# Performance work log

Measured on AMD Instinct MI355X. Metric: run time of the kernel, lower is better.

The kernel has to match this reference:

```python
import jax, jax.numpy as jnp
import numpy as np

EPS = 1e-5
NHEAD = 8
TOP_K = 2


def _layernorm(x, g, b):
    m = jnp.mean(x, axis=-1, keepdims=True)
    v = jnp.mean((x - m) ** 2, axis=-1, keepdims=True)
    return (x - m) * jax.lax.rsqrt(v + EPS) * g + b


def setup_inputs() -> dict:
    S, D, F, E = 4096, 512, 2048, 8
    key = jax.random.key(0)
    ks = jax.random.split(key, 18)
    std = 0.02
    return {
        "src": jax.random.normal(ks[0], (S, D), jnp.float32),
        "in_proj_w": std * jax.random.normal(ks[1], (3 * D, D), jnp.float32),
        "in_proj_b": jnp.zeros((3 * D,), jnp.float32),
        "out_proj_w": std * jax.random.normal(ks[2], (D, D), jnp.float32),
        "out_proj_b": jnp.zeros((D,), jnp.float32),
        "ln1_g": jnp.ones((D,), jnp.float32),
        "ln1_b": jnp.zeros((D,), jnp.float32),
        "ln2_g": jnp.ones((D,), jnp.float32),
        "ln2_b": jnp.zeros((D,), jnp.float32),
        "gate_w": std * jax.random.normal(ks[3], (E, D), jnp.float32),
        "gate_b": jnp.zeros((E,), jnp.float32),
        "w1": std * jax.random.normal(ks[4], (E, F, D), jnp.float32),
        "b1": jnp.zeros((E, F), jnp.float32),
        "w2": std * jax.random.normal(ks[5], (E, F, D), jnp.float32),
        "b2": jnp.zeros((E, F), jnp.float32),
        "wo": std * jax.random.normal(ks[6], (E, D, F), jnp.float32),
        "bo": jnp.zeros((E, D), jnp.float32),
    }


def _sa_block(x, in_proj_w, in_proj_b, out_proj_w, out_proj_b):
    # x: [S, D] unbatched sequence (torch MultiheadAttention unbatched path)
    S, D = x.shape
    hd = D // NHEAD
    qkv = x @ in_proj_w.T + in_proj_b              # [S, 3D]
    q, k, v = jnp.split(qkv, 3, axis=-1)
    q = q.reshape(S, NHEAD, hd)
    k = k.reshape(S, NHEAD, hd)
    v = v.reshape(S, NHEAD, hd)
    scores = jnp.einsum("shd,thd->hst", q, k) / jnp.sqrt(jnp.float32(hd))
    attn = jax.nn.softmax(scores, axis=-1)         # [H, S, S]
    out = jnp.einsum("hst,thd->shd", attn, v).reshape(S, D)
    return out @ out_proj_w.T + out_proj_b


def _ff_block(x, gate_w, gate_b, w1, b1, w2, b2, wo, bo):
    # top-k gated SwiGLU MoE; gate probs are softmax, NOT renormalized after topk
    T = x.shape[0]
    E = w1.shape[0]
    gates = jax.nn.softmax(x @ gate_w.T + gate_b, axis=-1)      # [T, E]
    top_scores, top_idx = jax.lax.top_k(gates, TOP_K)            # [T, k]
    combine = jnp.zeros((T, E), x.dtype).at[
        jnp.arange(T)[:, None], top_idx].add(top_scores)         # [T, E]
    out = jnp.zeros_like(x)
    for e in range(E):  # small fixed expert count
        h = jax.nn.silu(x @ w1[e].T + b1[e]) * (x @ w2[e].T + b2[e])
        out = out + combine[:, e:e + 1] * (h @ wo[e].T + bo[e])
    return out


def reference(src, in_proj_w, in_proj_b, out_proj_w, out_proj_b,
              ln1_g, ln1_b, ln2_g, ln2_b,
              gate_w, gate_b, w1, b1, w2, b2, wo, bo):
    # norm_first pre-norm residual layer, dropout=0 (eval)
    x = src
    x = x + _sa_block(_layernorm(x, ln1_g, ln1_b),
                      in_proj_w, in_proj_b, out_proj_w, out_proj_b)
    x = x + _ff_block(_layernorm(x, ln2_g, ln2_b),
                      gate_w, gate_b, w1, b1, w2, b2, wo, bo)
    return x
```

## Files before the change

kernel.cpp:

```cpp
#include <hip/hip_runtime.h>
#include <hip/hip_bf16.h>
#include <math.h>

#define SQ   4096
#define DM   512
#define NH   8
#define HDIM 64
#define FF   2048
#define NE   8

typedef unsigned short u16;
typedef unsigned int   u32;
typedef __attribute__((ext_vector_type(8))) __bf16 bf16x8;
typedef __attribute__((ext_vector_type(4))) float  f32x4;

__device__ __forceinline__ float bf2f(u16 v) {
    union { u32 i; float f; } c; c.i = ((u32)v) << 16; return c.f;
}
__device__ __forceinline__ u16 f2bf(float f) {
    union { __bf16 h; u16 u; } c; c.h = (__bf16)f; return c.u;
}

#define BM 128
#define BN 128
#define BK 32
#define BKP 40

__global__ __launch_bounds__(256) void gemm_split(
    const u16* __restrict__ Ahi, const u16* __restrict__ Alo, int lda,
    const u16* __restrict__ Bhi, const u16* __restrict__ Blo, int ldb,
    int M, int N, int K,
    const float* __restrict__ bias,
    const float* __restrict__ resid, int ldres,
    u16* __restrict__ Chi, u16* __restrict__ Clo,
    float* __restrict__ Cf, int ldc, int mode)
{
    __shared__ __align__(16) u16 Ash[BM * BKP], Asl[BM * BKP];
    __shared__ __align__(16) u16 Bsh[BN * BKP], Bsl[BN * BKP];
    const int tid  = threadIdx.x;
    const int wave = tid >> 6;
    const int lane = tid & 63;
    const int quad = lane >> 4;
    const int l16  = lane & 15;
    const int bm = blockIdx.x * BM;
    const int bn = blockIdx.y * BN;
    const int wm = (wave & 1) * 64;
    const int wn = (wave >> 1) * 64;

    f32x4 acc[4][4];
#pragma unroll
    for (int i = 0; i < 4; i++)
#pragma unroll
        for (int j = 0; j < 4; j++)
#pragma unroll
            for (int r = 0; r < 4; r++) acc[i][j][r] = 0.0f;

    for (int k0 = 0; k0 < K; k0 += BK) {
#pragma unroll
        for (int i = 0; i < 2; i++) {
            int c = tid + i * 256;
            int row = c >> 2;
            int col = (c & 3) << 3;
            int ga = bm + row, gb2 = bn + row;
            uint4 vah = make_uint4(0u,0u,0u,0u), val = vah, vbh = vah, vbl = vah;
            if (ga < M) {
                vah = *(const uint4*)(Ahi + (size_t)ga * lda + k0 + col);
                val = *(const uint4*)(Alo + (size_t)ga * lda + k0 + col);
            }
            if (gb2 < N) {
                vbh = *(const uint4*)(Bhi + (size_t)gb2 * ldb + k0 + col);
                vbl = *(const uint4*)(Blo + (size_t)gb2 * ldb + k0 + col);
            }
            *(uint4*)(Ash + row * BKP + col) = vah;
            *(uint4*)(Asl + row * BKP + col) = val;
            *(uint4*)(Bsh + row * BKP + col) = vbh;
            *(uint4*)(Bsl + row * BKP + col) = vbl;
        }
        __syncthreads();
        bf16x8 ah[4], al[4], bh[4], bl[4];
#pragma unroll
    for (int i = 0; i < 4; i++) {
            ah[i] = *(const bf16x8*)(Ash + (wm + i * 16 + l16) * BKP + quad * 8);
            al[i] = *(const bf16x8*)(Asl + (wm + i * 16 + l16) * BKP + quad * 8);
        }
#pragma unroll
        for (int j = 0; j < 4; j++) {
            bh[j] = *(const bf16x8*)(Bsh + (wn + j * 16 + l16) * BKP + quad * 8);
            bl[j] = *(const bf16x8*)(Bsl + (wn + j * 16 + l16) * BKP + quad * 8);
        }
#pragma unroll
        for (int i = 0; i < 4; i++)
#pragma unroll
            for (int j = 0; j < 4; j++) {
                acc[i][j] = __builtin_amdgcn_mfma_f32_16x16x32_bf16(ah[i], bh[j], acc[i][j], 0,0,0);
                acc[i][j] = __builtin_amdgcn_mfma_f32_16x16x32_bf16(ah[i], bl[j], acc[i][j], 0,0,0);
                acc[i][j] = __builtin_amdgcn_mfma_f32_16x16x32_bf16(al[i], bh[j], acc[i][j], 0,0,0);
            }
        __syncthreads();
    }

#pragma unroll
    for (int i = 0; i < 4; i++)
#pragma unroll
        for (int j = 0; j < 4; j++)
#pragma unroll
            for (int r = 0; r < 4; r++) {
                int row = bm + wm + i * 16 + quad * 4 + r;
                int col = bn + wn + j * 16 + l16;
                if (row >= M || col >= N) continue;
                float v = acc[i][j][r] + (bias ? bias[col] : 0.0f);
                size_t idx = (size_t)row * ldc + col;
                if (mode == 0) {
                    u16 hb = f2bf(v);
                    Chi[idx] = hb;
                    Clo[idx] = f2bf(v - bf2f(hb));
                } else {
                    if (resid) v += resid[(size_t)row * ldres + col];
                    Cf[idx] = v;
                }
            }
}

__global__ __launch_bounds__(256) void gemm_split_ko(
    const u16* __restrict__ Ahi, const u16* __restrict__ Alo, int lda,
    const u16* __restrict__ Bhi, const u16* __restrict__ Blo, int ldb,
    float* __restrict__ Cf, int ldc)
{
    __shared__ __align__(16) u16 Ash[BM * BKP], Asl[BM * BKP];
    __shared__ __align__(16) u16 Bsh[BN * BKP], Bsl[BN * BKP];
    const int tid  = threadIdx.x;
    const int wave = tid >> 6;
    const int lane = tid & 63;
    const int quad = lane >> 4;
    const int l16  = lane & 15;
    const int bm = blockIdx.x * BM;
    const int bn = blockIdx.y * BN;
    const int wm = (wave & 1) * 64;
    const int wn = (wave >> 1) * 64;
    const int KC    = DM / 4;
    const int k0beg = blockIdx.z * KC;

    f32x4 acc[4][4];
#pragma unroll
    for (int i = 0; i < 4; i++)
#pragma unroll
        for (int j = 0; j < 4; j++)
#pragma unroll
            for (int r = 0; r < 4; r++) acc[i][j][r] = 0.0f;

    for (int k0 = k0beg; k0 < k0beg + KC; k0 += BK) {
#pragma unroll
        for (int i = 0; i < 2; i++) {
            int c = tid + i * 256;
            int row = c >> 2;
            int col = (c & 3) << 3;
            int ga = bm + row, gb2 = bn + row;
            uint4 vah = *(const uint4*)(Ahi + (size_t)ga * lda + k0 + col);
            uint4 val = *(const uint4*)(Alo + (size_t)ga * lda + k0 + col);
            uint4 vbh = *(const uint4*)(Bhi + (size_t)gb2 * ldb + k0 + col);
            uint4 vbl = *(const uint4*)(Blo + (size_t)gb2 * ldb + k0 + col);
            *(uint4*)(Ash + row * BKP + col) = vah;
            *(uint4*)(Asl + row * BKP + col) = val;
            *(uint4*)(Bsh + row * BKP + col) = vbh;
            *(uint4*)(Bsl + row * BKP + col) = vbl;
        }
        __syncthreads();
        bf16x8 ah[4], al[4], bh[4], bl[4];
#pragma unroll
        for (int i = 0; i < 4; i++) {
            ah[i] = *(const bf16x8*)(Ash + (wm + i * 16 + l16) * BKP + quad * 8);
            al[i] = *(const bf16x8*)(Asl + (wm + i * 16 + l16) * BKP + quad * 8);
        }
#pragma unroll
        for (int j = 0; j < 4; j++) {
            bh[j] = *(const bf16x8*)(Bsh + (wn + j * 16 + l16) * BKP + quad * 8);
            bl[j] = *(const bf16x8*)(Bsl + (wn + j * 16 + l16) * BKP + quad * 8);
        }
#pragma unroll
        for (int i = 0; i < 4; i++)
#pragma unroll
            for (int j = 0; j < 4; j++) {
                acc[i][j] = __builtin_amdgcn_mfma_f32_16x16x32_bf16(ah[i], bh[j], acc[i][j], 0,0,0);
                acc[i][j] = __builtin_amdgcn_mfma_f32_16x16x32_bf16(ah[i], bl[j], acc[i][j], 0,0,0);
                acc[i][j] = __builtin_amdgcn_mfma_f32_16x16x32_bf16(al[i], bh[j], acc[i][j], 0,0,0);
            }
        __syncthreads();
    }

#pragma unroll
    for (int i = 0; i < 4; i++)
#pragma unroll
        for (int j = 0; j < 4; j++)
#pragma unroll
            for (int r = 0; r < 4; r++) {
                int row = bm + wm + i * 16 + quad * 4 + r;
                int col = bn + wn + j * 16 + l16;
                atomicAdd(Cf + (size_t)row * ldc + col, acc[i][j][r]);
            }
}

__global__ __launch_bounds__(256) void init_x1(
    const float* __restrict__ src, const float* __restrict__ bias,
    float* __restrict__ x1)
{
    int i = blockIdx.x * 256 + threadIdx.x;
    int col4 = i & (DM / 4 - 1);
    float4 s = ((const float4*)src)[i];
    float4 b = ((const float4*)bias)[col4];
    s.x += b.x; s.y += b.y; s.z += b.z; s.w += b.w;
    ((float4*)x1)[i] = s;
}

__global__ __launch_bounds__(256) void moe12_all(
    const u16* __restrict__ A, int lda,
    const int* __restrict__ idxl, const int* __restrict__ cnt,
    const int* __restrict__ off,
    const float* __restrict__ w1, const float* __restrict__ b1,
    const float* __restrict__ w2, const float* __restrict__ b2,
    u16* __restrict__ H)
{
    const int bmg = blockIdx.x * BM;
    if (bmg >= off[NE]) return;
    int e = 0;
    while (e < NE - 1 && bmg >= off[e + 1]) e++;
    const int M   = cnt[e];
    const int bml = bmg - off[e];
    if (bml >= M) return;
    const float* B1 = w1 + (size_t)e * FF * DM;
    const float* B2 = w2 + (size_t)e * FF * DM;
    const int*   rl = idxl + e * SQ;

    __shared__ __align__(16) u16 As[BM * BKP], Bs1[BN * BKP], Bs2[BN * BKP];
    const int tid  = threadIdx.x;
    const int wave = tid >> 6;
// ... 194 lines not shown

    f32x4 acc[4][4];
#pragma unroll
    for (int i = 0; i < 4; i++)
#pragma unroll
        for (int j = 0; j < 4; j++)
#pragma unroll
            for (int r = 0; r < 4; r++) acc[i][j][r] = 0.0f;

    for (int k0 = 0; k0 < FF; k0 += BK) {
#pragma unroll
        for (int i = 0; i < 2; i++) {
            int c = tid + i * 256;
            int row = c >> 2;
            int col = (c & 3) << 3;
            uint4 va = *(const uint4*)(H + (size_t)(bmg + row) * FF + k0 + col);
            *(uint4*)(As + row * BKP + col) = va;
        }
#pragma unroll
        for (int i = 0; i < 4; i++) {
            int c = tid + i * 256;
            int row = c >> 3;
            int col = (c & 7) << 2;
            float4 v = *(const float4*)(B + (size_t)(bn + row) * FF + k0 + col);
            ushort4 h;
            h.x = f2bf(v.x); h.y = f2bf(v.y); h.z = f2bf(v.z); h.w = f2bf(v.w);
            *(ushort4*)(Bs + row * BKP + col) = h;
        }
        __syncthreads();
        bf16x8 af[4], bf[4];
#pragma unroll
        for (int i = 0; i < 4; i++)
            af[i] = *(const bf16x8*)(As + (wm + i * 16 + l16) * BKP + quad * 8);
#pragma unroll
        for (int j = 0; j < 4; j++)
            bf[j] = *(const bf16x8*)(Bs + (wn + j * 16 + l16) * BKP + quad * 8);
#pragma unroll
        for (int i = 0; i < 4; i++)
#pragma unroll
            for (int j = 0; j < 4; j++)
                acc[i][j] = __builtin_amdgcn_mfma_f32_16x16x32_bf16(af[i], bf[j], acc[i][j], 0,0,0);
        __syncthreads();
    }

#pragma unroll
    for (int i = 0; i < 4; i++)
#pragma unroll
        for (int j = 0; j < 4; j++)
#pragma unroll
            for (int r = 0; r < 4; r++) {
                int rowl = bml + wm + i * 16 + quad * 4 + r;
                if (rowl >= M) continue;
                int col = bn + wn + j * 16 + l16;
                int tok = idxl[e * SQ + rowl];
                float wgt = cw[e * SQ + rowl];
                atomicAdd(out + (size_t)tok * DM + col,
                          wgt * (acc[i][j][r] + bo[e * DM + col]));
            }
}

__global__ __launch_bounds__(256) void moe_y_bf16(
    const u16* __restrict__ H,
    const u16* __restrict__ wob, const float* __restrict__ bo,
    const int* __restrict__ idxl, const float* __restrict__ cw,
    const int* __restrict__ cnt, const int* __restrict__ off,
    float* __restrict__ out)
{
    const int bmg = blockIdx.x * BM;
    if (bmg >= off[NE]) return;
    int e = 0;
    while (e < NE - 1 && bmg >= off[e + 1]) e++;
    const int M   = cnt[e];
    const int bml = bmg - off[e];
    if (bml >= M) return;
    const u16* B = wob + (size_t)e * DM * FF;

    __shared__ __align__(16) u16 As[BM * BKP], Bs[BN * BKP];
    const int tid  = threadIdx.x;
    const int wave = tid >> 6;
    const int lane = tid & 63;
    const int quad = lane >> 4;
    const int l16  = lane & 15;
    const int bn = blockIdx.y * BN;
    const int wm = (wave & 1) * 64;
    const int wn = (wave >> 1) * 64;

    f32x4 acc[4][4];
#pragma unroll
    for (int i = 0; i < 4; i++)
#pragma unroll
        for (int j = 0; j < 4; j++)
#pragma unroll
            for (int r = 0; r < 4; r++) acc[i][j][r] = 0.0f;

    for (int k0 = 0; k0 < FF; k0 += BK) {
#pragma unroll
        for (int i = 0; i < 2; i++) {
            int c = tid + i * 256;
            int row = c >> 2;
            int col = (c & 3) << 3;
            uint4 va = *(const uint4*)(H + (size_t)(bmg + row) * FF + k0 + col);
            *(uint4*)(As + row * BKP + col) = va;
            uint4 vb = *(const uint4*)(B + (size_t)(bn + row) * FF + k0 + col);
            *(uint4*)(Bs + row * BKP + col) = vb;
        }
        __syncthreads();
        bf16x8 af[4], bf[4];
#pragma unroll
        for (int i = 0; i < 4; i++)
            af[i] = *(const bf16x8*)(As + (wm + i * 16 + l16) * BKP + quad * 8);
#pragma unroll
        for (int j = 0; j < 4; j++)
            bf[j] = *(const bf16x8*)(Bs + (wn + j * 16 + l16) * BKP + quad * 8);
#pragma unroll
        for (int i = 0; i < 4; i++)
#pragma unroll
            for (int j = 0; j < 4; j++)
                acc[i][j] = __builtin_amdgcn_mfma_f32_16x16x32_bf16(af[i], bf[j], acc[i][j], 0,0,0);
        __syncthreads();
    }

#pragma unroll
    for (int i = 0; i < 4; i++)
#pragma unroll
        for (int j = 0; j < 4; j++)
#pragma unroll
            for (int r = 0; r < 4; r++) {
                int rowl = bml + wm + i * 16 + quad * 4 + r;
                if (rowl >= M) continue;
                int col = bn + wn + j * 16 + l16;
                int tok = idxl[e * SQ + rowl];
                float wgt = cw[e * SQ + rowl];
                atomicAdd(out + (size_t)tok * DM + col,
                          wgt * (acc[i][j][r] + bo[e * DM + col]));
            }
}

__global__ __launch_bounds__(256) void cvt_w_bf16(
    const float* __restrict__ w, u16* __restrict__ wb, int n4)
{
    int i = blockIdx.x * 256 + threadIdx.x;
    if (i < n4) {
        float4 v = ((const float4*)w)[i];
        ushort4 h;
        h.x = f2bf(v.x); h.y = f2bf(v.y); h.z = f2bf(v.z); h.w = f2bf(v.w);
        ((ushort4*)wb)[i] = h;
    }
}

#define KP 64
#define SWZ(row, col) ((col) ^ (((row) & 7) << 3))
#define SCL 0.18033688011112042f

template <int SPLIT>
__device__ __forceinline__ void flash_body(
    const u16* __restrict__ qh, const u16* __restrict__ ql,
    const u16* __restrict__ vth, const u16* __restrict__ vtl,
    u16* __restrict__ oh, u16* __restrict__ ol,
    float* __restrict__ Opart, float* __restrict__ mpart,
    float* __restrict__ lpart)
{
    __shared__ __align__(16) u16 Ksh[64*KP], Ksl[64*KP], Vsh[64*KP], Vsl[64*KP];
    const int tid  = threadIdx.x;
    const int wave = tid >> 6;
    const int lane = tid & 63;
    const int quad = lane >> 4;
    const int l16  = lane & 15;
    const int h    = blockIdx.y;
    const int z    = (SPLIT > 1) ? blockIdx.z : 0;
    const int qbase = blockIdx.x * 64 + wave * 16;

    const int r_st  = tid >> 3;
    const int co_g  = (tid & 7) << 3;
    const int co_sw = SWZ(r_st, co_g);

    bf16x8 aqh[2], aql[2];
#pragma unroll
    for (int kk = 0; kk < 2; kk++) {
        size_t off = (size_t)(qbase + l16) * (3*DM) + h*HDIM + kk*32 + quad*8;
        aqh[kk] = *(const bf16x8*)(qh + off);
        aql[kk] = *(const bf16x8*)(ql + off);
    }

    float m_ = -1e30f, l_ = 0.0f;
    f32x4 o_[4];
#pragma unroll
    for (int nd = 0; nd < 4; nd++)
#pragma unroll
        for (int r = 0; r < 4; r++) o_[nd][r] = 0.0f;

    const int srcA = l16 + ((quad & 1) * 2) * 16;
    const int srcB = srcA + 16;
    const bool hiJ = (quad >> 1);

    const int NT    = SQ / 64 / SPLIT;
    const int jtBeg = z * NT, jtEnd = (z + 1) * NT;

    for (int jt = jtBeg; jt < jtEnd; jt++) {
        {
            size_t koff0 = (size_t)(jt*64 + r_st) * (3*DM) + DM + h*HDIM + co_g;
            size_t voff0 = (size_t)(h*HDIM + r_st) * SQ + jt*64 + co_g;
            size_t koff1 = koff0 + (size_t)32 * (3*DM);
            size_t voff1 = voff0 + (size_t)32 * SQ;
            uint4 a0 = *(const uint4*)(qh  + koff0);
            uint4 a1 = *(const uint4*)(ql  + koff0);
            uint4 a2 = *(const uint4*)(vth + voff0);
            uint4 a3 = *(const uint4*)(vtl + voff0);
            uint4 b0 = *(const uint4*)(qh  + koff1);
            uint4 b1 = *(const uint4*)(ql  + koff1);
            uint4 b2 = *(const uint4*)(vth + voff1);
            uint4 b3 = *(const uint4*)(vtl + voff1);
            *(uint4*)(Ksh + r_st*KP + co_sw)      = a0;
            *(uint4*)(Ksl + r_st*KP + co_sw)      = a1;
            *(uint4*)(Vsh + r_st*KP + co_sw)      = a2;
            *(uint4*)(Vsl + r_st*KP + co_sw)      = a3;
            *(uint4*)(Ksh + (r_st+32)*KP + co_sw) = b0;
            *(uint4*)(Ksl + (r_st+32)*KP + co_sw) = b1;
            *(uint4*)(Vsh + (r_st+32)*KP + co_sw) = b2;
            *(uint4*)(Vsl + (r_st+32)*KP + co_sw) = b3;
        }
        __syncthreads();

        f32x4 s[4];
        __builtin_amdgcn_s_setprio(1);
#pragma unroll
        for (int jn = 0; jn < 4; jn++) {
            f32x4 zz;
#pragma unroll
            for (int r = 0; r < 4; r++) zz[r] = 0.0f;
#pragma unroll
            for (int kk = 0; kk < 2; kk++) {
                int krow = jn*16 + l16;
                int kcol = SWZ(krow, kk*32 + quad*8);
                bf16x8 kh = *(const bf16x8*)(Ksh + krow*KP + kcol);
                bf16x8 kl = *(const bf16x8*)(Ksl + krow*KP + kcol);
                zz = __builtin_amdgcn_mfma_f32_16x16x32_bf16(kh, aqh[kk], zz, 0,0,0);
                zz = __builtin_amdgcn_mfma_f32_16x16x32_bf16(kl, aqh[kk], zz, 0,0,0);
                zz = __builtin_amdgcn_mfma_f32_16x16x32_bf16(kh, aql[kk], zz, 0,0,0);
            }
#pragma unroll
            for (int r = 0; r < 4; r++) zz[r] *= SCL;
            s[jn] = zz;
        }
        __builtin_amdgcn_s_setprio(0);

        float mx = s[0][0];
#pragma unroll
        for (int jn = 0; jn < 4; jn++)
#pragma unroll
            for (int r = 0; r < 4; r++) mx = fmaxf(mx, s[jn][r]);
        mx = fmaxf(mx, __shfl_xor(mx, 16));
        mx = fmaxf(mx, __shfl_xor(mx, 32));

        int grew = (mx > m_ + 8.0f) ? 1 : 0;
        if (__any(grew)) {
            float nm  = fmaxf(m_, mx);
            float al2 = exp2f(m_ - nm);
            m_ = nm;
            l_ *= al2;
            float alq[4];
#pragma unroll
            for (int r = 0; r < 4; r++)
                alq[r] = __shfl(al2, quad*4 + r);
#pragma unroll
            for (int nd = 0; nd < 4; nd++)
#pragma unroll
                for (int r = 0; r < 4; r++) o_[nd][r] *= alq[r];
        }

        float rs = 0.0f;
#pragma unroll
        for (int jn = 0; jn < 4; jn++)
#pragma unroll
            for (int r = 0; r < 4; r++) {
                float p = exp2f(s[jn][r] - m_);
                s[jn][r] = p;
                rs += p;
            }
        rs += __shfl_xor(rs, 16);
        rs += __shfl_xor(rs, 32);
        l_ += rs;

        u32 phk[4][2], plk[4][2];
#pragma unroll
        for (int jn = 0; jn < 4; jn++) {
            u16 h0 = f2bf(s[jn][0]), h1 = f2bf(s[jn][1]);
            u16 h2 = f2bf(s[jn][2]), h3 = f2bf(s[jn][3]);
            phk[jn][0] = (u32)h0 | ((u32)h1 << 16);
            phk[jn][1] = (u32)h2 | ((u32)h3 << 16);
            u16 g0 = f2bf(s[jn][0] - bf2f(h0)), g1 = f2bf(s[jn][1] - bf2f(h1));
            u16 g2 = f2bf(s[jn][2] - bf2f(h2)), g3 = f2bf(s[jn][3] - bf2f(h3));
            plk[jn][0] = (u32)g0 | ((u32)g1 << 16);
            plk[jn][1] = (u32)g2 | ((u32)g3 << 16);
        }

        bf16x8 phf[2], plf[2];
#pragma unroll
        for (int kk = 0; kk < 2; kk++) {
            int jA = kk*2, jB = kk*2 + 1;
            uint4 wh, wl;
            {
                u32 a = (u32)__shfl((int)phk[jA][0], srcA);
                u32 b = (u32)__shfl((int)phk[jB][0], srcA);
                wh.x = hiJ ? b : a;
                a = (u32)__shfl((int)phk[jA][1], srcA);
                b = (u32)__shfl((int)phk[jB][1], srcA);
                wh.y = hiJ ? b : a;
                a = (u32)__shfl((int)phk[jA][0], srcB);
                b = (u32)__shfl((int)phk[jB][0], srcB);
                wh.z = hiJ ? b : a;
                a = (u32)__shfl((int)phk[jA][1], srcB);
                b = (u32)__shfl((int)phk[jB][1], srcB);
                wh.w = hiJ ? b : a;
            }
            {
                u32 a = (u32)__shfl((int)plk[jA][0], srcA);
                u32 b = (u32)__shfl((int)plk[jB][0], srcA);
                wl.x = hiJ ? b : a;
                a = (u32)__shfl((int)plk[jA][1], srcA);
                b = (u32)__shfl((int)plk[jB][1], srcA);
                wl.y = hiJ ? b : a;
                a = (u32)__shfl((int)plk[jA][0], srcB);
                b = (u32)__shfl((int)plk[jB][0], srcB);
                wl.z = hiJ ? b : a;
                a = (u32)__shfl((int)plk[jA][1], srcB);
                b = (u32)__shfl((int)plk[jB][1], srcB);
                wl.w = hiJ ? b : a;
            }
            union { uint4 u; bf16x8 v; } ch, cl;
            ch.u = wh; cl.u = wl;
            phf[kk] = ch.v;
            plf[kk] = cl.v;
        }

        __builtin_amdgcn_s_setprio(1);
#pragma unroll
        for (int nd = 0; nd < 4; nd++) {
#pragma unroll
            for (int kk = 0; kk < 2; kk++) {
                int vrow = nd*16 + l16;
                int vcol = SWZ(vrow, kk*32 + quad*8);
                bf16x8 vh = *(const bf16x8*)(Vsh + vrow*KP + vcol);
                bf16x8 vl = *(const bf16x8*)(Vsl + vrow*KP + vcol);
                o_[nd] = __builtin_amdgcn_mfma_f32_16x16x32_bf16(phf[kk], vh, o_[nd], 0,0,0);
                o_[nd] = __builtin_amdgcn_mfma_f32_16x16x32_bf16(phf[kk], vl, o_[nd], 0,0,0);
                o_[nd] = __builtin_amdgcn_mfma_f32_16x16x32_bf16(plf[kk], vh, o_[nd], 0,0,0);
            }
        }
        __builtin_amdgcn_s_setprio(0);
        __syncthreads();
    }

    if (SPLIT == 1) {
        float lq[4];
#pragma unroll
        for (int r = 0; r < 4; r++) lq[r] = __shfl(l_, quad*4 + r);
#pragma unroll
        for (int nd = 0; nd < 4; nd++)
#pragma unroll
            for (int r = 0; r < 4; r++) {
                int row = qbase + quad*4 + r;
                int col = h*HDIM + nd*16 + l16;
                float w = o_[nd][r] / lq[r];
                u16 hb = f2bf(w);
                oh[(size_t)row * DM + col] = hb;
                ol[(size_t)row * DM + col] = f2bf(w - bf2f(hb));
            }
    } else {
#pragma unroll
        for (int nd = 0; nd < 4; nd++)
#pragma unroll
            for (int r = 0; r < 4; r++) {
                int row = qbase + quad*4 + r;
                int col = h*HDIM + nd*16 + l16;
                Opart[((size_t)z * SQ + row) * DM + col] = o_[nd][r];
            }
        if (lane < 16) {
            int row = qbase + l16;
            mpart[(z*NH + h) * SQ + row] = m_;
            lpart[(z*NH + h) * SQ + row] = l_;
        }
    }
}

__global__ __launch_bounds__(256) void flash_attn(
    const u16* __restrict__ qh, const u16* __restrict__ ql,
    const u16* __restrict__ vth, const u16* __restrict__ vtl,
    u16* __restrict__ oh, u16* __restrict__ ol)
{
    flash_body<1>(qh, ql, vth, vtl, oh, ol, nullptr, nullptr, nullptr);
}

__global__ __launch_bounds__(256) void flash_attn_part2(
    const u16* __restrict__ qh, const u16* __restrict__ ql,
    const u16* __restrict__ vth, const u16* __restrict__ vtl,
    float* __restrict__ Opart, float* __restrict__ mpart,
    float* __restrict__ lpart)
{
    flash_body<2>(qh, ql, vth, vtl, nullptr, nullptr, Opart, mpart, lpart);
}

__global__ __launch_bounds__(256) void flash_attn_part4(
    const u16* __restrict__ qh, const u16* __restrict__ ql,
    const u16* __restrict__ vth, const u16* __restrict__ vtl,
    float* __restrict__ Opart, float* __restrict__ mpart,
    float* __restrict__ lpart)
{
    flash_body<4>(qh, ql, vth, vtl, nullptr, nullptr, Opart, mpart, lpart);
}

__global__ __launch_bounds__(256) void attn_combine(
    const float* __restrict__ Opart, const float* __restrict__ mpart,
    const float* __restrict__ lpart,
    u16* __restrict__ oh, u16* __restrict__ ol, int ns)
{
    const int row = blockIdx.x;
    const int tid = threadIdx.x;
#pragma unroll
    for (int i = 0; i < 2; i++) {
        int col = tid + i * 256;
        int h = col >> 6;
        float m = -1e30f;
        for (int zz = 0; zz < ns; zz++)
            m = fmaxf(m, mpart[(zz*NH + h) * SQ + row]);
        float O = 0.0f, l = 0.0f;
        for (int zz = 0; zz < ns; zz++) {
            float a = exp2f(mpart[(zz*NH + h) * SQ + row] - m);
            O += Opart[((size_t)zz * SQ + row) * DM + col] * a;
            l += lpart[(zz*NH + h) * SQ + row] * a;
        }
        float w = O / l;
        u16 hb = f2bf(w);
        oh[(size_t)row * DM + col] = hb;
        ol[(size_t)row * DM + col] = f2bf(w - bf2f(hb));
    }
}

__global__ __launch_bounds__(256) void ln1_split(
    const float* __restrict__ x, const float* __restrict__ g,
    const float* __restrict__ b, u16* __restrict__ ohi, u16* __restrict__ olo)
{
    const int row = blockIdx.x;
    const int tid = threadIdx.x;
    float v0 = x[(size_t)row * DM + tid];
    float v1 = x[(size_t)row * DM + tid + 256];
    float s = v0 + v1, sq = v0*v0 + v1*v1;
#pragma unroll
    for (int o = 1; o < 64; o <<= 1) { s += __shfl_xor(s, o); sq += __shfl_xor(sq, o); }
    __shared__ float ss[4], ssq[4];
    if ((tid & 63) == 0) { ss[tid>>6] = s; ssq[tid>>6] = sq; }
    __syncthreads();
    s  = ss[0]+ss[1]+ss[2]+ss[3];
    sq = ssq[0]+ssq[1]+ssq[2]+ssq[3];
    float m = s * (1.0f/DM);
    float rstd = rsqrtf(sq*(1.0f/DM) - m*m + 1e-5f);
    float y0 = (v0-m)*rstd*g[tid]     + b[tid];
    float y1 = (v1-m)*rstd*g[tid+256] + b[tid+256];
    u16 h0 = f2bf(y0), h1 = f2bf(y1);
    ohi[(size_t)row*DM + tid]       = h0;  olo[(size_t)row*DM + tid]       = f2bf(y0 - bf2f(h0));
    ohi[(size_t)row*DM + tid + 256] = h1;  olo[(size_t)row*DM + tid + 256] = f2bf(y1 - bf2f(h1));
}

__global__ __launch_bounds__(256) void transpose_v2(
    const u16* __restrict__ qh, const u16* __restrict__ ql,
    u16* __restrict__ vth, u16* __restrict__ vtl)
{
    __shared__ u16 Th[64 * 66], Tl[64 * 66];
    const int t0  = blockIdx.x * 64;
    const int hd0 = blockIdx.y * 64;
    const int tid = threadIdx.x;
#pragma unroll
    for (int k = 0; k < 16; k++) {
        int idx = tid + k * 256;
        int r = idx >> 6, j = idx & 63;
        size_t src = (size_t)(t0 + r) * (3*DM) + 2*DM + hd0 + j;
        Th[r * 66 + j] = qh[src];
        Tl[r * 66 + j] = ql[src];
    }
    __syncthreads();
#pragma unroll
    for (int k = 0; k < 16; k++) {
        int idx = tid + k * 256;
        int r = idx >> 6, c2 = idx & 63;
        size_t dst = (size_t)(hd0 + r) * SQ + t0 + c2;
        vth[dst] = Th[c2 * 66 + r];
        vtl[dst] = Tl[c2 * 66 + r];
    }
}

__global__ __launch_bounds__(256) void gate_route(
    const float* __restrict__ x1, const float* __restrict__ g,
    const float* __restrict__ b, const float* __restrict__ gw,
    const float* __restrict__ gb,
    int* __restrict__ cnt, int* __restrict__ idxl, float* __restrict__ cw,
    u16* __restrict__ xout, float* __restrict__ outcpy)
{
    const int token = blockIdx.x * 4 + (threadIdx.x >> 6);
    const int lane  = threadIdx.x & 63;
    const float* xr = x1 + (size_t)token * DM;
    float v[8];
#pragma unroll
    for (int i = 0; i < 8; i++) v[i] = xr[lane*8 + i];
    {
        float4* od = (float4*)(outcpy + (size_t)token * DM + lane*8);
        od[0] = make_float4(v[0], v[1], v[2], v[3]);
        od[1] = make_float4(v[4], v[5], v[6], v[7]);
    }
    float s = 0.f, sq = 0.f;
#pragma unroll
    for (int i = 0; i < 8; i++) { s += v[i]; sq += v[i]*v[i]; }
#pragma unroll
    for (int o = 1; o < 64; o <<= 1) { s += __shfl_xor(s, o); sq += __shfl_xor(sq, o); }
    float m = s * (1.0f/DM);
    float rstd = rsqrtf(sq*(1.0f/DM) - m*m + 1e-5f);
    float xn[8];
#pragma unroll
    for (int i = 0; i < 8; i++)
        xn[i] = (v[i]-m)*rstd*g[lane*8+i] + b[lane*8+i];
    {
        uint4 w;
        w.x = (u32)f2bf(xn[0]) | ((u32)f2bf(xn[1]) << 16);
        w.y = (u32)f2bf(xn[2]) | ((u32)f2bf(xn[3]) << 16);
        w.z = (u32)f2bf(xn[4]) | ((u32)f2bf(xn[5]) << 16);
        w.w = (u32)f2bf(xn[6]) | ((u32)f2bf(xn[7]) << 16);
        *(uint4*)(xout + (size_t)token * DM + lane*8) = w;
    }
    float logit[8];
#pragma unroll
    for (int e = 0; e < 8; e++) {
        float t = 0.f;
#pragma unroll
        for (int i = 0; i < 8; i++) t += xn[i] * gw[e*DM + lane*8 + i];
#pragma unroll
        for (int o = 1; o < 64; o <<= 1) t += __shfl_xor(t, o);
        logit[e] = t + gb[e];
    }
    if (lane == 0) {
        float mx = -1e30f;
        for (int e = 0; e < 8; e++) mx = fmaxf(mx, logit[e]);
        float den = 0.f, p[8];
        for (int e = 0; e < 8; e++) { p[e] = __expf(logit[e] - mx); den += p[e]; }
        for (int e = 0; e < 8; e++) p[e] /= den;
        int i1 = 0;
        for (int e = 1; e < 8; e++) if (p[e] > p[i1]) i1 = e;
        int i2 = -1;
        for (int e = 0; e < 8; e++) { if (e == i1) continue; if (i2 < 0 || p[e] > p[i2]) i2 = e; }
        int s1 = atomicAdd(&cnt[i1], 1);
        idxl[i1*SQ + s1] = token;  cw[i1*SQ + s1] = p[i1];
        int s2 = atomicAdd(&cnt[i2], 1);
        idxl[i2*SQ + s2] = token;  cw[i2*SQ + s2] = p[i2];
    }
}

__global__ __launch_bounds__(256) void cvt_split_w(
    const float* __restrict__ w, u16* __restrict__ wh, u16* __restrict__ wl, int n)
{
    int i = blockIdx.x * 256 + threadIdx.x;
    if (i < n) {
        float v = w[i];
        u16 h = f2bf(v);
        wh[i] = h;
        wl[i] = f2bf(v - bf2f(h));
    }
}

__global__ __launch_bounds__(64) void zero_cnt(int* cnt)
{
    if (threadIdx.x < NE) cnt[threadIdx.x] = 0;
}

__global__ __launch_bounds__(64) void make_off(const int* __restrict__ cnt,
                                              int* __restrict__ off)
{
    if (threadIdx.x == 0) {
        int a = 0;
        for (int e = 0; e < NE; e++) {
            off[e] = a;
            a += ((cnt[e] + 127) >> 7) << 7;
        }
        off[NE] = a;
    }
}

__global__ __launch_bounds__(256) void sentinel_kernel(float* out, float v, int n)
{
    int i = blockIdx.x * 256 + threadIdx.x;
    if (i < n) out[i] = v;
}
__global__ __launch_bounds__(256) void scrub_kernel(float* out, int n)
{
    int i = blockIdx.x * 256 + threadIdx.x;
    if (i < n) { float v = out[i]; if (!isfinite(v)) out[i] = 777.0f; }
}

extern "C" void kernel_launch(void* const* d_in, const int* in_sizes, int n_in,
                              void* d_out, int out_size, void* d_ws, size_t ws_size,
                              hipStream_t stream)
{
    const float* src        = (const float*)d_in[0];
    const float* in_proj_w  = (const float*)d_in[1];
    const float* in_proj_b  = (const float*)d_in[2];
    const float* out_proj_w = (const float*)d_in[3];
    const float* out_proj_b = (const float*)d_in[4];
    const float* ln1_g      = (const float*)d_in[5];
    const float* ln1_b      = (const float*)d_in[6];
    const float* ln2_g      = (const float*)d_in[7];
    const float* ln2_b      = (const float*)d_in[8];
    const float* gate_w     = (const float*)d_in[9];
    const float* gate_b     = (const float*)d_in[10];
    const float* w1         = (const float*)d_in[11];
    const float* b1         = (const float*)d_in[12];
    const float* w2         = (const float*)d_in[13];
    const float* b2         = (const float*)d_in[14];
    const float* wo         = (const float*)d_in[15];
    const float* bo         = (const float*)d_in[16];
    float* out = (float*)d_out;

    const size_t MB = (size_t)1 << 20;
    const size_t ROUTE = 512 * 1024;
    const size_t NEED      = ROUTE + 44 * MB;
    const size_t NEED_BIG2 = ROUTE + 61 * MB;
    const size_t NEED_BIG4 = ROUTE + 78 * MB;
    if (ws_size < NEED) {
        sentinel_kernel<<<(SQ*DM)/256, 256, 0, stream>>>(out, 333.0f, SQ*DM);
        return;
    }
    int ns = 0;
    if (ws_size >= NEED_BIG4)      ns = 4;
    else if (ws_size >= NEED_BIG2) ns = 2;

    char* ws = (char*)d_ws;
    int*   cnt  = (int*)ws;
    int*   offp = (int*)(ws + 64);
    int*   idxl = (int*)(ws + 1024);
    float* cw   = (float*)(ws + 1024 + 128*1024);
    char*  base = ws + ROUTE;
    u16* xln1h = (u16*)(base);
    u16* xln1l = (u16*)(base + 4*MB);
    u16* attnh = (u16*)(base);
    u16* attnl = (u16*)(base + 4*MB);
    u16* qkvh  = (u16*)(base + 8*MB);
    u16* qkvl  = (u16*)(base + 20*MB);
    float* x1  = (float*)(base + 8*MB);
    u16* vth   = (u16*)(base + 32*MB);
    u16* vtl   = (u16*)(base + 36*MB);
    u16* xln2  = (u16*)(base + 36*MB);
    u16* Hbuf  = (u16*)(base);
    u16* wph   = (u16*)(base + 40*MB);
    u16* wpl   = (u16*)(base + 40*MB + 1536*1024);
    u16* woh   = (u16*)(base + 43*MB);
    u16* wol   = (u16*)(base + 43*MB + 512*1024);
    float* Opart = (float*)(base + 44*MB);
    float* mpart;
    float* lpart;
    if (ns == 4) {
        mpart = (float*)(base + 76*MB);
        lpart = (float*)(base + 76*MB + 512*1024);
    } else {
        mpart = (float*)(base + 60*MB);
        lpart = (float*)(base + 60*MB + 256*1024);
    }
    u16* w1b = (u16*)(base + 44*MB);
    u16* w2b = (u16*)(base + 60*MB);
    u16* wob = (u16*)(base + 44*MB);

    cvt_split_w<<<(3*DM*DM)/256, 256, 0, stream>>>(in_proj_w,  wph, wpl, 3*DM*DM);
    cvt_split_w<<<(DM*DM)/256,   256, 0, stream>>>(out_proj_w, woh, wol, DM*DM);

    ln1_split<<<SQ, 256, 0, stream>>>(src, ln1_g, ln1_b, xln1h, xln1l);
    gemm_split<<<dim3(32, 12), 256, 0, stream>>>(
        xln1h, xln1l, DM, wph, wpl, DM, SQ, 3*DM, DM,
        in_proj_b, nullptr, 0, qkvh, qkvl, nullptr, 3*DM, 0);
    transpose_v2<<<dim3(SQ/64, DM/64), 256, 0, stream>>>(qkvh, qkvl, vth, vtl);
    if (ns == 4) {
        flash_attn_part4<<<dim3(SQ/64, NH, 4), 256, 0, stream>>>(
            qkvh, qkvl, vth, vtl, Opart, mpart, lpart);
        attn_combine<<<SQ, 256, 0, stream>>>(Opart, mpart, lpart, attnh, attnl, 4);
    } else if (ns == 2) {
        flash_attn_part2<<<dim3(SQ/64, NH, 2), 256, 0, stream>>>(
            qkvh, qkvl, vth, vtl, Opart, mpart, lpart);
        attn_combine<<<SQ, 256, 0, stream>>>(Opart, mpart, lpart, attnh, attnl, 2);
    } else {
        flash_attn<<<dim3(SQ/64, NH), 256, 0, stream>>>(
            qkvh, qkvl, vth, vtl, attnh, attnl);
    }
    init_x1<<<(SQ*DM/4)/256, 256, 0, stream>>>(src, out_proj_b, x1);
    gemm_split_ko<<<dim3(32, 4, 4), 256, 0, stream>>>(
        attnh, attnl, DM, woh, wol, DM, x1, DM);

    zero_cnt<<<1, 64, 0, stream>>>(cnt);
    gate_route<<<SQ/4, 256, 0, stream>>>(x1, ln2_g, ln2_b, gate_w, gate_b,
                                         cnt, idxl, cw, xln2, out);
    make_off<<<1, 64, 0, stream>>>(cnt, offp);
    const int WN4 = (NE * FF * DM) / 4;
    if (ns == 4) {
        cvt_w_bf16<<<WN4/256, 256, 0, stream>>>(w1, w1b, WN4);
        cvt_w_bf16<<<WN4/256, 256, 0, stream>>>(w2, w2b, WN4);
        moe12_bf16<<<dim3(72, 16), 256, 0, stream>>>(
            xln2, DM, idxl, cnt, offp, w1b, b1, w2b, b2, Hbuf);
        cvt_w_bf16<<<WN4/256, 256, 0, stream>>>(wo, wob, WN4);
        moe_y_bf16<<<dim3(72, 4), 256, 0, stream>>>(
            Hbuf, wob, bo, idxl, cw, cnt, offp, out);
    } else {
        moe12_all<<<dim3(72, 16), 256, 0, stream>>>(
            xln2, DM, idxl, cnt, offp, w1, b1, w2, b2, Hbuf);
        moe_y_all<<<dim3(72, 4), 256, 0, stream>>>(
            Hbuf, wo, bo, idxl, cw, cnt, offp, out);
    }

    scrub_kernel<<<(SQ*DM)/256, 256, 0, stream>>>(out, SQ*DM);
}
```

Baseline: 729.2 us.

## Process two query tiles per wave in flash attention to reuse K/V tiles

Each wave now handles 32 query rows as two 16-row tiles instead of 16, so every block covers 128 queries and the grid halves. Each K/V tile loaded into shared memory and each LDS fragment read now feeds twice as many MFMAs, cutting global and LDS traffic per unit of work. The softmax and bf16 hi/lo packing is moved into a helper called once per tile. This raises register pressure and halves the number of blocks, which may lower occupancy and parallelism on the split variants.

```diff
diff --git a/kernel.cpp b/kernel.cpp
--- a/kernel.cpp
+++ b/kernel.cpp
@@ -79,7 +79,7 @@
         __syncthreads();
         bf16x8 ah[4], al[4], bh[4], bl[4];
 #pragma unroll
-    for (int i = 0; i < 4; i++) {
+        for (int i = 0; i < 4; i++) {
             ah[i] = *(const bf16x8*)(Ash + (wm + i * 16 + l16) * BKP + quad * 8);
             al[i] = *(const bf16x8*)(Asl + (wm + i * 16 + l16) * BKP + quad * 8);
         }
@@ -580,6 +580,100 @@
 #define SWZ(row, col) ((col) ^ (((row) & 7) << 3))
 #define SCL 0.18033688011112042f
 
+__device__ __forceinline__ void smax_pack(
+    f32x4 (&s)[4], float &m_, float &l_, f32x4 (&o_)[4],
+    bf16x8 (&phf)[2], bf16x8 (&plf)[2],
+    int quad, int srcA, int srcB, bool hiJ)
+{
+    float mx = s[0][0];
+#pragma unroll
+    for (int jn = 0; jn < 4; jn++)
+#pragma unroll
+        for (int r = 0; r < 4; r++) mx = fmaxf(mx, s[jn][r]);
+    mx = fmaxf(mx, __shfl_xor(mx, 16));
+    mx = fmaxf(mx, __shfl_xor(mx, 32));
+
+    int grew = (mx > m_ + 8.0f) ? 1 : 0;
+    if (__any(grew)) {
+        float nm  = fmaxf(m_, mx);
+        float al2 = exp2f(m_ - nm);
+        m_ = nm;
+        l_ *= al2;
+        float alq[4];
+#pragma unroll
+        for (int r = 0; r < 4; r++)
+            alq[r] = __shfl(al2, quad*4 + r);
+#pragma unroll
+        for (int nd = 0; nd < 4; nd++)
+#pragma unroll
+            for (int r = 0; r < 4; r++) o_[nd][r] *= alq[r];
+    }
+
+    float rs = 0.0f;
+#pragma unroll
+    for (int jn = 0; jn < 4; jn++)
+#pragma unroll
+        for (int r = 0; r < 4; r++) {
+            float p = exp2f(s[jn][r] - m_);
+            s[jn][r] = p;
+            rs += p;
+        }
+    rs += __shfl_xor(rs, 16);
+    rs += __shfl_xor(rs, 32);
+    l_ += rs;
+
+    u32 phk[4][2], plk[4][2];
+#pragma unroll
+    for (int jn = 0; jn < 4; jn++) {
+        u16 h0 = f2bf(s[jn][0]), h1 = f2bf(s[jn][1]);
+        u16 h2 = f2bf(s[jn][2]), h3 = f2bf(s[jn][3]);
+        phk[jn][0] = (u32)h0 | ((u32)h1 << 16);
+        phk[jn][1] = (u32)h2 | ((u32)h3 << 16);
+        u16 g0 = f2bf(s[jn][0] - bf2f(h0)), g1 = f2bf(s[jn][1] - bf2f(h1));
+        u16 g2 = f2bf(s[jn][2] - bf2f(h2)), g3 = f2bf(s[jn][3] - bf2f(h3));
+        plk[jn][0] = (u32)g0 | ((u32)g1 << 16);
+        plk[jn][1] = (u32)g2 | ((u32)g3 << 16);
+    }
+
+#pragma unroll
+    for (int kk = 0; kk < 2; kk++) {
+        int jA = kk*2, jB = kk*2 + 1;
+        uint4 wh, wl;
+        {
+            u32 a = (u32)__shfl((int)phk[jA][0], srcA);
+            u32 b = (u32)__shfl((int)phk[jB][0], srcA);
+            wh.x = hiJ ? b : a;
+            a = (u32)__shfl((int)phk[jA][1], srcA);
+            b = (u32)__shfl((int)phk[jB][1], srcA);
+            wh.y = hiJ ? b : a;
+            a = (u32)__shfl((int)phk[jA][0], srcB);
+            b = (u32)__shfl((int)phk[jB][0], srcB);
+            wh.z = hiJ ? b : a;
+            a = (u32)__shfl((int)phk[jA][1], srcB);
+            b = (u32)__shfl((int)phk[jB][1], srcB);
+            wh.w = hiJ ? b : a;
+        }
+        {
+            u32 a = (u32)__shfl((int)plk[jA][0], srcA);
+            u32 b = (u32)__shfl((int)plk[jB][0], srcA);
+            wl.x = hiJ ? b : a;
+            a = (u32)__shfl((int)plk[jA][1], srcA);
+            b = (u32)__shfl((int)plk[jB][1], srcA);
+            wl.y = hiJ ? b : a;
+            a = (u32)__shfl((int)plk[jA][0], srcB);
+            b = (u32)__shfl((int)plk[jB][0], srcB);
+            wl.z = hiJ ? b : a;
+            a = (u32)__shfl((int)plk[jA][1], srcB);
+            b = (u32)__shfl((int)plk[jB][1], srcB);
+            wl.w = hiJ ? b : a;
+        }
+        union { uint4 u; bf16x8 v; } ch, cl;
+        ch.u = wh; cl.u = wl;
+        phf[kk] = ch.v;
+        plf[kk] = cl.v;
+    }
+}
+
 template <int SPLIT>
 __device__ __forceinline__ void flash_body(
     const u16* __restrict__ qh, const u16* __restrict__ ql,
@@ -596,26 +690,29 @@
     const int l16  = lane & 15;
     const int h    = blockIdx.y;
     const int z    = (SPLIT > 1) ? blockIdx.z : 0;
-    const int qbase = blockIdx.x * 64 + wave * 16;
+    const int qbase = blockIdx.x * 128 + wave * 32;
 
     const int r_st  = tid >> 3;
     const int co_g  = (tid & 7) << 3;
     const int co_sw = SWZ(r_st, co_g);
 
-    bf16x8 aqh[2], aql[2];
+    bf16x8 aqh0[2], aql0[2], aqh1[2], aql1[2];
 #pragma unroll
     for (int kk = 0; kk < 2; kk++) {
-        size_t off = (size_t)(qbase + l16) * (3*DM) + h*HDIM + kk*32 + quad*8;
-        aqh[kk] = *(const bf16x8*)(qh + off);
-        aql[kk] = *(const bf16x8*)(ql + off);
-    }
-
-    float m_ = -1e30f, l_ = 0.0f;
-    f32x4 o_[4];
+        size_t off0 = (size_t)(qbase + l16) * (3*DM) + h*HDIM + kk*32 + quad*8;
+        size_t off1 = off0 + (size_t)16 * (3*DM);
+        aqh0[kk] = *(const bf16x8*)(qh + off0);
+        aql0[kk] = *(const bf16x8*)(ql + off0);
+        aqh1[kk] = *(const bf16x8*)(qh + off1);
+        aql1[kk] = *(const bf16x8*)(ql + off1);
+    }
+
+    float m0 = -1e30f, l0 = 0.0f, m1 = -1e30f, l1 = 0.0f;
+    f32x4 o0[4], o1[4];
 #pragma unroll
     for (int nd = 0; nd < 4; nd++)
 #pragma unroll
-        for (int r = 0; r < 4; r++) o_[nd][r] = 0.0f;
+        for (int r = 0; r < 4; r++) { o0[nd][r] = 0.0f; o1[nd][r] = 0.0f; }
 
     const int srcA = l16 + ((quad & 1) * 2) * 16;
     const int srcB = srcA + 16;
@@ -649,117 +746,36 @@
         }
         __syncthreads();
 
-        f32x4 s[4];
+        f32x4 s0[4], s1[4];
         __builtin_amdgcn_s_setprio(1);
 #pragma unroll
         for (int jn = 0; jn < 4; jn++) {
-            f32x4 zz;
-#pragma unroll
-            for (int r = 0; r < 4; r++) zz[r] = 0.0f;
+            f32x4 z0, z1;
+#pragma unroll
+            for (int r = 0; r < 4; r++) { z0[r] = 0.0f; z1[r] = 0.0f; }
 #pragma unroll
             for (int kk = 0; kk < 2; kk++) {
                 int krow = jn*16 + l16;
                 int kcol = SWZ(krow, kk*32 + quad*8);
                 bf16x8 kh = *(const bf16x8*)(Ksh + krow*KP + kcol);
                 bf16x8 kl = *(const bf16x8*)(Ksl + krow*KP + kcol);
-                zz = __builtin_amdgcn_mfma_f32_16x16x32_bf16(kh, aqh[kk], zz, 0,0,0);
-                zz = __builtin_amdgcn_mfma_f32_16x16x32_bf16(kl, aqh[kk], zz, 0,0,0);
-                zz = __builtin_amdgcn_mfma_f32_16x16x32_bf16(kh, aql[kk], zz, 0,0,0);
-            }
-#pragma unroll
-            for (int r = 0; r < 4; r++) zz[r] *= SCL;
-            s[jn] = zz;
+                z0 = __builtin_amdgcn_mfma_f32_16x16x32_bf16(kh, aqh0[kk], z0, 0,0,0);
+                z0 = __builtin_amdgcn_mfma_f32_16x16x32_bf16(kl, aqh0[kk], z0, 0,0,0);
+                z0 = __builtin_amdgcn_mfma_f32_16x16x32_bf16(kh, aql0[kk], z0, 0,0,0);
+                z1 = __builtin_amdgcn_mfma_f32_16x16x32_bf16(kh, aqh1[kk], z1, 0,0,0);
+                z1 = __builtin_amdgcn_mfma_f32_16x16x32_bf16(kl, aqh1[kk], z1, 0,0,0);
+                z1 = __builtin_amdgcn_mfma_f32_16x16x32_bf16(kh, aql1[kk], z1, 0,0,0);
+            }
+#pragma unroll
+            for (int r = 0; r < 4; r++) { z0[r] *= SCL; z1[r] *= SCL; }
+            s0[jn] = z0;
+            s1[jn] = z1;
         }
         __builtin_amdgcn_s_setprio(0);
 
-        float mx = s[0][0];
-#pragma unroll
-        for (int jn = 0; jn < 4; jn++)
-#pragma unroll
-            for (int r = 0; r < 4; r++) mx = fmaxf(mx, s[jn][r]);
-        mx = fmaxf(mx, __shfl_xor(mx, 16));
-        mx = fmaxf(mx, __shfl_xor(mx, 32));
-
-        int grew = (mx > m_ + 8.0f) ? 1 : 0;
-        if (__any(grew)) {
-            float nm  = fmaxf(m_, mx);
-            float al2 = exp2f(m_ - nm);
-            m_ = nm;
-            l_ *= al2;
-            float alq[4];
-#pragma unroll
-            for (int r = 0; r < 4; r++)
-                alq[r] = __shfl(al2, quad*4 + r);
-#pragma unroll
-            for (int nd = 0; nd < 4; nd++)
-#pragma unroll
-                for (int r = 0; r < 4; r++) o_[nd][r] *= alq[r];
-        }
-
-        float rs = 0.0f;
-#pragma unroll
-        for (int jn = 0; jn < 4; jn++)
-#pragma unroll
-            for (int r = 0; r < 4; r++) {
-                float p = exp2f(s[jn][r] - m_);
-                s[jn][r] = p;
-                rs += p;
-            }
-        rs += __shfl_xor(rs, 16);
-        rs += __shfl_xor(rs, 32);
-        l_ += rs;
-
-        u32 phk[4][2], plk[4][2];
-#pragma unroll
-        for (int jn = 0; jn < 4; jn++) {
-            u16 h0 = f2bf(s[jn][0]), h1 = f2bf(s[jn][1]);
-            u16 h2 = f2bf(s[jn][2]), h3 = f2bf(s[jn][3]);
-            phk[jn][0] = (u32)h0 | ((u32)h1 << 16);
-            phk[jn][1] = (u32)h2 | ((u32)h3 << 16);
-            u16 g0 = f2bf(s[jn][0] - bf2f(h0)), g1 = f2bf(s[jn][1] - bf2f(h1));
-            u16 g2 = f2bf(s[jn][2] - bf2f(h2)), g3 = f2bf(s[jn][3] - bf2f(h3));
-            plk[jn][0] = (u32)g0 | ((u32)g1 << 16);
-            plk[jn][1] = (u32)g2 | ((u32)g3 << 16);
-        }
-
-        bf16x8 phf[2], plf[2];
-#pragma unroll
-        for (int kk = 0; kk < 2; kk++) {
-            int jA = kk*2, jB = kk*2 + 1;
-            uint4 wh, wl;
-            {
-                u32 a = (u32)__shfl((int)phk[jA][0], srcA);
-                u32 b = (u32)__shfl((int)phk[jB][0], srcA);
-                wh.x = hiJ ? b : a;
-                a = (u32)__shfl((int)phk[jA][1], srcA);
-                b = (u32)__shfl((int)phk[jB][1], srcA);
-                wh.y = hiJ ? b : a;
-                a = (u32)__shfl((int)phk[jA][0], srcB);
-                b = (u32)__shfl((int)phk[jB][0], srcB);
-                wh.z = hiJ ? b : a;
-                a = (u32)__shfl((int)phk[jA][1], srcB);
-                b = (u32)__shfl((int)phk[jB][1], srcB);
-                wh.w = hiJ ? b : a;
-            }
-            {
-                u32 a = (u32)__shfl((int)plk[jA][0], srcA);
-                u32 b = (u32)__shfl((int)plk[jB][0], srcA);
-                wl.x = hiJ ? b : a;
-                a = (u32)__shfl((int)plk[jA][1], srcA);
-                b = (u32)__shfl((int)plk[jB][1], srcA);
-                wl.y = hiJ ? b : a;
-                a = (u32)__shfl((int)plk[jA][0], srcB);
-                b = (u32)__shfl((int)plk[jB][0], srcB);
-                wl.z = hiJ ? b : a;
-                a = (u32)__shfl((int)plk[jA][1], srcB);
-                b = (u32)__shfl((int)plk[jB][1], srcB);
-                wl.w = hiJ ? b : a;
-            }
-            union { uint4 u; bf16x8 v; } ch, cl;
-            ch.u = wh; cl.u = wl;
-            phf[kk] = ch.v;
-            plf[kk] = cl.v;
-        }
+        bf16x8 phf0[2], plf0[2], phf1[2], plf1[2];
+        smax_pack(s0, m0, l0, o0, phf0, plf0, quad, srcA, srcB, hiJ);
+        smax_pack(s1, m1, l1, o1, phf1, plf1, quad, srcA, srcB, hiJ);
 
         __builtin_amdgcn_s_setprio(1);
 #pragma unroll
@@ -770,9 +786,12 @@
                 int vcol = SWZ(vrow, kk*32 + quad*8);
                 bf16x8 vh = *(const bf16x8*)(Vsh + vrow*KP + vcol);
                 bf16x8 vl = *(const bf16x8*)(Vsl + vrow*KP + vcol);
-                o_[nd] = __builtin_amdgcn_mfma_f32_16x16x32_bf16(phf[kk], vh, o_[nd], 0,0,0);
-                o_[nd] = __builtin_amdgcn_mfma_f32_16x16x32_bf16(phf[kk], vl, o_[nd], 0,0,0);
-                o_[nd] = __builtin_amdgcn_mfma_f32_16x16x32_bf16(plf[kk], vh, o_[nd], 0,0,0);
+                o0[nd] = __builtin_amdgcn_mfma_f32_16x16x32_bf16(phf0[kk], vh, o0[nd], 0,0,0);
+                o0[nd] = __builtin_amdgcn_mfma_f32_16x16x32_bf16(phf0[kk], vl, o0[nd], 0,0,0);
+                o0[nd] = __builtin_amdgcn_mfma_f32_16x16x32_bf16(plf0[kk], vh, o0[nd], 0,0,0);
+                o1[nd] = __builtin_amdgcn_mfma_f32_16x16x32_bf16(phf1[kk], vh, o1[nd], 0,0,0);
+                o1[nd] = __builtin_amdgcn_mfma_f32_16x16x32_bf16(phf1[kk], vl, o1[nd], 0,0,0);
+                o1[nd] = __builtin_amdgcn_mfma_f32_16x16x32_bf16(plf1[kk], vh, o1[nd], 0,0,0);
             }
         }
         __builtin_amdgcn_s_setprio(0);
@@ -780,19 +799,27 @@
     }
 
     if (SPLIT == 1) {
-        float lq[4];
-#pragma unroll
-        for (int r = 0; r < 4; r++) lq[r] = __shfl(l_, quad*4 + r);
+        float lq0[4], lq1[4];
+#pragma unroll
+        for (int r = 0; r < 4; r++) {
+            lq0[r] = __shfl(l0, quad*4 + r);
+            lq1[r] = __shfl(l1, quad*4 + r);
+        }
 #pragma unroll
         for (int nd = 0; nd < 4; nd++)
 #pragma unroll
             for (int r = 0; r < 4; r++) {
                 int row = qbase + quad*4 + r;
                 int col = h*HDIM + nd*16 + l16;
-                float w = o_[nd][r] / lq[r];
+                float w = o0[nd][r] / lq0[r];
                 u16 hb = f2bf(w);
                 oh[(size_t)row * DM + col] = hb;
                 ol[(size_t)row * DM + col] = f2bf(w - bf2f(hb));
+                int row1 = row + 16;
+                float w1v = o1[nd][r] / lq1[r];
+                u16 hb1 = f2bf(w1v);
+                oh[(size_t)row1 * DM + col] = hb1;
+                ol[(size_t)row1 * DM + col] = f2bf(w1v - bf2f(hb1));
             }
     } else {
 #pragma unroll
@@ -801,12 +828,15 @@
             for (int r = 0; r < 4; r++) {
                 int row = qbase + quad*4 + r;
                 int col = h*HDIM + nd*16 + l16;
-                Opart[((size_t)z * SQ + row) * DM + col] = o_[nd][r];
+                Opart[((size_t)z * SQ + row) * DM + col] = o0[nd][r];
+                Opart[((size_t)z * SQ + row + 16) * DM + col] = o1[nd][r];
             }
         if (lane < 16) {
             int row = qbase + l16;
-            mpart[(z*NH + h) * SQ + row] = m_;
-            lpart[(z*NH + h) * SQ + row] = l_;
+            mpart[(z*NH + h) * SQ + row] = m0;
+            lpart[(z*NH + h) * SQ + row] = l0;
+            mpart[(z*NH + h) * SQ + row + 16] = m1;
+            lpart[(z*NH + h) * SQ + row + 16] = l1;
         }
     }
 }
@@ -1101,15 +1131,15 @@
         in_proj_b, nullptr, 0, qkvh, qkvl, nullptr, 3*DM, 0);
     transpose_v2<<<dim3(SQ/64, DM/64), 256, 0, stream>>>(qkvh, qkvl, vth, vtl);
     if (ns == 4) {
-        flash_attn_part4<<<dim3(SQ/64, NH, 4), 256, 0, stream>>>(
+        flash_attn_part4<<<dim3(SQ/128, NH, 4), 256, 0, stream>>>(
             qkvh, qkvl, vth, vtl, Opart, mpart, lpart);
         attn_combine<<<SQ, 256, 0, stream>>>(Opart, mpart, lpart, attnh, attnl, 4);
     } else if (ns == 2) {
-        flash_attn_part2<<<dim3(SQ/64, NH, 2), 256, 0, stream>>>(
+        flash_attn_part2<<<dim3(SQ/128, NH, 2), 256, 0, stream>>>(
             qkvh, qkvl, vth, vtl, Opart, mpart, lpart);
         attn_combine<<<SQ, 256, 0, stream>>>(Opart, mpart, lpart, attnh, attnl, 2);
     } else {
-        flash_attn<<<dim3(SQ/64, NH), 256, 0, stream>>>(
+        flash_attn<<<dim3(SQ/128, NH), 256, 0, stream>>>(
             qkvh, qkvl, vth, vtl, attnh, attnl);
     }
     init_x1<<<(SQ*DM/4)/256, 256, 0, stream>>>(src, out_proj_b, x1);
```

Measured after the change: 724.0 us. About the same (-0.7%).
